# Performance work log

Hardware: AMD Instinct MI355X
Metric: run time of the kernel (lower is better)

The kernel has to match this reference:

```python
import jax, jax.numpy as jnp
import numpy as np

# Dims: B=batch, N_IN=input capsules, D_IN=input capsule dim,
#       J=output capsules (nb_capsules), C=output capsule dim (capsule_size)
B, N_IN, D_IN, J, C = 32, 2048, 16, 64, 32
ITERS = 5
EPS = 1e-7  # K.epsilon()


def squash(v):
    # Keras code: vector += eps; norm = sum(v^2, -1, keepdims); v * norm/(1+norm)/sqrt(norm)
    v = v + EPS
    n = jnp.sum(v * v, axis=-1, keepdims=True)
    return v * (n / (1.0 + n) / jnp.sqrt(n))


def setup_inputs() -> dict:
    key = jax.random.key(0)
    k1, k2 = jax.random.split(key)
    x = jax.random.normal(k1, (B, N_IN, D_IN, 1), dtype=jnp.float32)
    # glorot_uniform over fan_in=D_IN (last axis), fan_out=C
    limit = float(np.sqrt(6.0 / (D_IN + C)))
    W = jax.random.uniform(k2, (N_IN, J, C, D_IN), dtype=jnp.float32,
                           minval=-limit, maxval=limit)
    return {"x": x, "W": W}


def reference(x, W):
    # x: (B, N_IN, D_IN, 1) -> u: (B, N_IN, D_IN)
    u = x[..., 0]
    # Prediction vectors u_hat[b,i,j] = W[i,j] @ u[b,i] : (B, N_IN, J, C)
    u_hat = jnp.einsum('bid,ijcd->bijc', u, W)
    # Routing logits b_ij: (B, N_IN, J)
    b = jnp.zeros(u_hat.shape[:3], dtype=u_hat.dtype)
    v = None
    for i in range(ITERS):
        c = jax.nn.softmax(b, axis=1)              # softmax over input capsules (axis=1 in source)
        s = jnp.einsum('bij,bijc->bjc', c, u_hat)   # weighted sum over i -> (B, J, C)
        v = squash(s)                                # squash over capsule vector dim C
        if i < ITERS - 1:
            # agreement update: b += <v_j, u_hat_ij>
            b = b + jnp.einsum('bjc,bijc->bij', v, u_hat)
    # match compute_output_shape (B, nb_capsules, capsule_size, 1)
    return v[..., None]
```

## Files before the change

kernel.cpp:

```cpp
#include <hip/hip_runtime.h>
#include <hip/hip_bf16.h>

#define B_ 32
#define N_ 2048
#define D_ 16
#define J_ 64
#define C_ 32
#define NCHUNK 32
#define ICHUNK 64
#define IPW    16

typedef __attribute__((ext_vector_type(8)))  short short8;
typedef __attribute__((ext_vector_type(4)))  short s16x4;
typedef __attribute__((ext_vector_type(16))) float f32x16;
typedef __attribute__((ext_vector_type(4)))  float f32x4;

using bf16_t = __hip_bfloat16;

__global__ __launch_bounds__(256) void prep_u_kernel(const float* __restrict__ x,
                                                     bf16_t* __restrict__ ut) {
  int t  = blockIdx.x * 256 + threadIdx.x;
  int d4 = t & 3;
  int bi = t >> 2;
  int b  = bi & 31;
  int i  = bi >> 5;
  f32x4 xv = *(const f32x4*)(x + ((size_t)(b * N_ + i) * D_ + d4 * 4));
  union { s16x4 v; bf16_t h[4]; } o;
  o.h[0] = __float2bfloat16(xv.x);
  o.h[1] = __float2bfloat16(xv.y);
  o.h[2] = __float2bfloat16(xv.z);
  o.h[3] = __float2bfloat16(xv.w);
  *(s16x4*)(ut + (size_t)(i * B_ + b) * D_ + d4 * 4) = o.v;
}

template<int MODE>
__global__ __launch_bounds__(256) void pass_kernel(
    const float*  __restrict__ Wf,
    const bf16_t* __restrict__ Wb,
    bf16_t*       __restrict__ Wbo,
    const bf16_t* __restrict__ ut,
    const float*  __restrict__ V,
    float*        __restrict__ PS,
    float*        __restrict__ PZ)
{
  constexpr bool UNIFORM = (MODE == 0 || MODE == 2);
  constexpr bool READF32 = (MODE != 1);
  constexpr bool STOREB  = (MODE == 0);

  const int tid  = threadIdx.x;
  const int w    = tid >> 6;
  const int lane = tid & 63;
  const int half = lane >> 5;
  const int lc   = lane & 31;

  const int j  = blockIdx.x / NCHUNK;
  const int ch = blockIdx.x % NCHUNK;

  int crow[16];
#pragma unroll
  for (int r = 0; r < 16; ++r) crow[r] = (r & 3) + 4 * half + 8 * (r >> 2);

  float Vreg[16];
  if (!UNIFORM) {
#pragma unroll
    for (int r = 0; r < 16; ++r) Vreg[r] = V[(lc * J_ + j) * C_ + crow[r]];
  }

  float S[16];
#pragma unroll
  for (int r = 0; r < 16; ++r) S[r] = 0.f;
  float zacc = 0.f;

  const int ibase = ch * ICHUNK + w * IPW;
  const int frag_off = lc * D_ + half * 8;

  const f32x16 zeroacc = {0,0,0,0,0,0,0,0,0,0,0,0,0,0,0,0};

  for (int t = 0; t < IPW; ++t) {
    const int i = ibase + t;
    short8 ufrag = *(const short8*)(ut + (size_t)i * (B_ * D_) + frag_off);
    short8 wfrag;
    const size_t tile = ((size_t)i * J_ + j) * (C_ * D_);
    if (READF32) {
      const float* wp = Wf + tile + frag_off;
      f32x4 w0 = *(const f32x4*)(wp);
      f32x4 w1 = *(const f32x4*)(wp + 4);
      union { short8 v; bf16_t h[8]; } cv;
      cv.h[0] = __float2bfloat16(w0.x);
      cv.h[1] = __float2bfloat16(w0.y);
      cv.h[2] = __float2bfloat16(w0.z);
      cv.h[3] = __float2bfloat16(w0.w);
      cv.h[4] = __float2bfloat16(w1.x);
      cv.h[5] = __float2bfloat16(w1.y);
      cv.h[6] = __float2bfloat16(w1.z);
      cv.h[7] = __float2bfloat16(w1.w);
      wfrag = cv.v;
      if (STOREB) *(short8*)(Wbo + tile + frag_off) = wfrag;
    } else {
      wfrag = *(const short8*)(Wb + tile + frag_off);
    }

    f32x16 acc = __builtin_amdgcn_mfma_f32_32x32x16_bf16(wfrag, ufrag, zeroacc, 0, 0, 0);

    if (UNIFORM) {
#pragma unroll
      for (int r = 0; r < 16; ++r) S[r] += acc[r];
    } else {
      float ph = 0.f;
#pragma unroll
      for (int r = 0; r < 16; ++r) ph = fmaf(Vreg[r], acc[r], ph);
      ph += __shfl_xor(ph, 32);
      float e = __expf(ph);
      zacc += e;
#pragma unroll
      for (int r = 0; r < 16; ++r) S[r] = fmaf(e, acc[r], S[r]);
    }
  }

  __shared__ float S_lds[4 * 32 * 33];
  __shared__ float Z_lds[4 * 32];
#pragma unroll
  for (int r = 0; r < 16; ++r)
    S_lds[w * 1056 + lc * 33 + crow[r]] = S[r];
  if (!half)
    Z_lds[w * 32 + lc] = UNIFORM ? (float)IPW : zacc;
  __syncthreads();

  const size_t pbase = (size_t)blockIdx.x * 1024;
  for (int e = tid; e < 1024; e += 256) {
    int b = e >> 5, c = e & 31;
    PS[pbase + e] = S_lds[b * 33 + c] + S_lds[1056 + b * 33 + c] +
                    S_lds[2112 + b * 33 + c] + S_lds[3168 + b * 33 + c];
  }
  if (tid < 32)
    PZ[(size_t)blockIdx.x * 32 + tid] =
        Z_lds[tid] + Z_lds[32 + tid] + Z_lds[64 + tid] + Z_lds[96 + tid];
}

__global__ __launch_bounds__(256) void combine_kernel(
    const float* __restrict__ PS, const float* __restrict__ PZ,
    float* __restrict__ V, float* __restrict__ out, int first, int last)
{
  int t  = blockIdx.x * 256 + threadIdx.x;
  int c  = t & 31;
  int bj = t >> 5;
  int b  = bj >> 6;
  int j  = bj & 63;
  float s = 0.f, zz = 0.f;
#pragma unroll
  for (int ch = 0; ch < NCHUNK; ++ch) {
    s  += PS[(size_t)(j * NCHUNK + ch) * 1024 + b * 32 + c];
    zz += PZ[(j * NCHUNK + ch) * 32 + b];
  }
  float sv = s / zz + 1e-7f;
  float n = sv * sv;
  n += __shfl_xor(n, 1);
  n += __shfl_xor(n, 2);
  n += __shfl_xor(n, 4);
  n += __shfl_xor(n, 8);
  n += __shfl_xor(n, 16);
  float f = n / ((1.f + n) * sqrtf(n));
  float v = sv * f;
  float Vn = first ? v : (V[t] + v);
  V[t] = Vn;
  if (last) out[t] = v;
}

extern "C" void kernel_launch(void* const* d_in, const int* in_sizes, int n_in,
                              void* d_out, int out_size, void* d_ws, size_t ws_size,
                              hipStream_t stream)
{
  const float* x  = (const float*)d_in[0];
  const float* Wf = (const float*)d_in[1];
  float* out = (float*)d_out;
  char* ws = (char*)d_ws;

  const size_t SZ_WB = (size_t)N_ * J_ * C_ * D_ * 2;
  const size_t SZ_UT = (size_t)N_ * B_ * D_ * 2;
  const size_t SZ_V  = (size_t)B_ * J_ * C_ * 4;
  const size_t SZ_PS = (size_t)J_ * NCHUNK * B_ * C_ * 4;
  const size_t SZ_PZ = (size_t)J_ * NCHUNK * B_ * 4;

  const bool big = ws_size >= SZ_WB + SZ_UT + SZ_V + SZ_PS + SZ_PZ;
  size_t off = big ? SZ_WB : 0;
  bf16_t* Wb = (bf16_t*)ws;
  bf16_t* ut = (bf16_t*)(ws + off); off += SZ_UT;
  float*  V  = (float*)(ws + off);  off += SZ_V;
  float*  PS = (float*)(ws + off);  off += SZ_PS;
  float*  PZ = (float*)(ws + off);

  prep_u_kernel<<<dim3((N_ * B_ * 4) / 256), dim3(256), 0, stream>>>(x, ut);

  dim3 gA(J_ * NCHUNK), blk(256), gB((B_ * J_ * C_) / 256);
  if (big) {
    pass_kernel<0><<<gA, blk, 0, stream>>>(Wf, nullptr, Wb, ut, nullptr, PS, PZ);
    combine_kernel<<<gB, blk, 0, stream>>>(PS, PZ, V, out, 1, 0);
    for (int it = 1; it < 5; ++it) {
      pass_kernel<1><<<gA, blk, 0, stream>>>(nullptr, Wb, nullptr, ut, V, PS, PZ);
      combine_kernel<<<gB, blk, 0, stream>>>(PS, PZ, V, out, 0, it == 4 ? 1 : 0);
    }
  } else {
    pass_kernel<2><<<gA, blk, 0, stream>>>(Wf, nullptr, nullptr, ut, nullptr, PS, PZ);
    combine_kernel<<<gB, blk, 0, stream>>>(PS, PZ, V, out, 1, 0);
    for (int it = 1; it < 5; ++it) {
      pass_kernel<3><<<gA, blk, 0, stream>>>(Wf, nullptr, nullptr, ut, V, PS, PZ);
      combine_kernel<<<gB, blk, 0, stream>>>(PS, PZ, V, out, 0, it == 4 ? 1 : 0);
    }
  }
}
```

Measured before the change: 512.5 us.

## Quantize W and u to int8 with per-tile scales and use i8 MFMA

The first pass now quantizes each W[i,j] 32x16 tile to int8 with a per-tile absmax scale and stores it to the workspace. The prep kernel quantizes each u[b,i] vector to int8 with a per-vector scale. Later routing passes stream the int8 weights, half the bytes of the previous bf16 copy, run i8 MFMA, and rescale the accumulators in fp32. This targets the memory-bandwidth cost of re-reading W every iteration, in exchange for lower precision and extra scale loads and conversions.

```diff
diff --git a/kernel.cpp b/kernel.cpp
--- a/kernel.cpp
+++ b/kernel.cpp
@@ -14,38 +14,59 @@
 typedef __attribute__((ext_vector_type(4)))  short s16x4;
 typedef __attribute__((ext_vector_type(16))) float f32x16;
 typedef __attribute__((ext_vector_type(4)))  float f32x4;
+typedef __attribute__((ext_vector_type(16))) int   i32x16;
+typedef __attribute__((ext_vector_type(2)))  long  longx2;
 
 using bf16_t = __hip_bfloat16;
 
 __global__ __launch_bounds__(256) void prep_u_kernel(const float* __restrict__ x,
-                                                     bf16_t* __restrict__ ut) {
-  int t  = blockIdx.x * 256 + threadIdx.x;
-  int d4 = t & 3;
-  int bi = t >> 2;
-  int b  = bi & 31;
-  int i  = bi >> 5;
-  f32x4 xv = *(const f32x4*)(x + ((size_t)(b * N_ + i) * D_ + d4 * 4));
-  union { s16x4 v; bf16_t h[4]; } o;
-  o.h[0] = __float2bfloat16(xv.x);
-  o.h[1] = __float2bfloat16(xv.y);
-  o.h[2] = __float2bfloat16(xv.z);
-  o.h[3] = __float2bfloat16(xv.w);
-  *(s16x4*)(ut + (size_t)(i * B_ + b) * D_ + d4 * 4) = o.v;
+                                                     bf16_t* __restrict__ ut,
+                                                     signed char* __restrict__ uq,
+                                                     float* __restrict__ su) {
+  int t = blockIdx.x * 256 + threadIdx.x;
+  int b = t & 31;
+  int i = t >> 5;
+  const float* xp = x + (size_t)(b * N_ + i) * D_;
+  float v[16];
+  *(f32x4*)(v)      = *(const f32x4*)(xp);
+  *(f32x4*)(v + 4)  = *(const f32x4*)(xp + 4);
+  *(f32x4*)(v + 8)  = *(const f32x4*)(xp + 8);
+  *(f32x4*)(v + 12) = *(const f32x4*)(xp + 12);
+
+  float m = 0.f;
+#pragma unroll
+  for (int k = 0; k < 16; ++k) m = fmaxf(m, fabsf(v[k]));
+  m = fmaxf(m, 1e-20f);
+  float inv = 127.0f / m;
+  union { longx2 l2; signed char c[16]; } pk;
+#pragma unroll
+  for (int k = 0; k < 16; ++k) pk.c[k] = (signed char)__float2int_rn(v[k] * inv);
+  *(longx2*)(uq + (size_t)t * D_) = pk.l2;
+  su[t] = m * (1.0f / 127.0f);
+
+  union { short8 s; bf16_t h[8]; } o0, o1;
+#pragma unroll
+  for (int k = 0; k < 8; ++k) { o0.h[k] = __float2bfloat16(v[k]); o1.h[k] = __float2bfloat16(v[8 + k]); }
+  *(short8*)(ut + (size_t)t * D_)     = o0.s;
+  *(short8*)(ut + (size_t)t * D_ + 8) = o1.s;
 }
 
 template<int MODE>
 __global__ __launch_bounds__(256) void pass_kernel(
-    const float*  __restrict__ Wf,
-    const bf16_t* __restrict__ Wb,
-    bf16_t*       __restrict__ Wbo,
-    const bf16_t* __restrict__ ut,
-    const float*  __restrict__ V,
-    float*        __restrict__ PS,
-    float*        __restrict__ PZ)
+    const float*        __restrict__ Wf,
+    const signed char*  __restrict__ Wq,
+    signed char*        __restrict__ Wqo,
+    float*              __restrict__ SWo,
+    const float*        __restrict__ SW,
+    const signed char*  __restrict__ uq,
+    const float*        __restrict__ su,
+    const bf16_t*       __restrict__ ut,
+    const float*        __restrict__ V,
+    float*              __restrict__ PS,
+    float*              __restrict__ PZ)
 {
   constexpr bool UNIFORM = (MODE == 0 || MODE == 2);
-  constexpr bool READF32 = (MODE != 1);
-  constexpr bool STOREB  = (MODE == 0);
+  constexpr bool INT8    = (MODE == 0 || MODE == 1);
 
   const int tid  = threadIdx.x;
   const int w    = tid >> 6;
@@ -74,14 +95,68 @@
   const int ibase = ch * ICHUNK + w * IPW;
   const int frag_off = lc * D_ + half * 8;
 
-  const f32x16 zeroacc = {0,0,0,0,0,0,0,0,0,0,0,0,0,0,0,0};
-
-  for (int t = 0; t < IPW; ++t) {
-    const int i = ibase + t;
-    short8 ufrag = *(const short8*)(ut + (size_t)i * (B_ * D_) + frag_off);
-    short8 wfrag;
-    const size_t tile = ((size_t)i * J_ + j) * (C_ * D_);
-    if (READF32) {
+  if constexpr (INT8) {
+    const i32x16 zi = {0,0,0,0,0,0,0,0,0,0,0,0,0,0,0,0};
+    for (int t = 0; t < IPW; ++t) {
+      const int i = ibase + t;
+      long ul = *(const long*)(uq + (size_t)i * (B_ * D_) + frag_off);
+      const size_t tile = ((size_t)i * J_ + j) * (C_ * D_);
+      long wl;
+      float sw_i;
+      if constexpr (MODE == 0) {
+        const float* wp = Wf + tile + frag_off;
+        f32x4 w0 = *(const f32x4*)(wp);
+        f32x4 w1 = *(const f32x4*)(wp + 4);
+        float wv[8] = {w0.x, w0.y, w0.z, w0.w, w1.x, w1.y, w1.z, w1.w};
+        float m = 0.f;
+#pragma unroll
+        for (int k = 0; k < 8; ++k) m = fmaxf(m, fabsf(wv[k]));
+        m = fmaxf(m, __shfl_xor(m, 1));
+        m = fmaxf(m, __shfl_xor(m, 2));
+        m = fmaxf(m, __shfl_xor(m, 4));
+        m = fmaxf(m, __shfl_xor(m, 8));
+        m = fmaxf(m, __shfl_xor(m, 16));
+        m = fmaxf(m, __shfl_xor(m, 32));
+        m = fmaxf(m, 1e-20f);
+        float qs = 127.0f / m;
+        union { long l; signed char c[8]; } pk;
+#pragma unroll
+        for (int k = 0; k < 8; ++k) pk.c[k] = (signed char)__float2int_rn(wv[k] * qs);
+        wl = pk.l;
+        sw_i = m * (1.0f / 127.0f);
+        *(long*)(Wqo + tile + frag_off) = wl;
+        if (lane == 0) SWo[(size_t)i * J_ + j] = sw_i;
+      } else {
+        wl = *(const long*)(Wq + tile + frag_off);
+        sw_i = SW[(size_t)i * J_ + j];
+      }
+      const float s = sw_i * su[i * B_ + lc];
+
+      i32x16 iacc = __builtin_amdgcn_mfma_i32_32x32x16_i8(wl, ul, zi, 0, 0, 0);
+
+      if constexpr (UNIFORM) {
+#pragma unroll
+        for (int r = 0; r < 16; ++r) S[r] = fmaf(s, (float)iacc[r], S[r]);
+      } else {
+        float af[16];
+        float ph = 0.f;
+#pragma unroll
+        for (int r = 0; r < 16; ++r) { af[r] = (float)iacc[r]; ph = fmaf(Vreg[r], af[r], ph); }
+        ph *= s;
+        ph += __shfl_xor(ph, 32);
+        float e = __expf(ph);
+        zacc += e;
+        float es = e * s;
+#pragma unroll
+        for (int r = 0; r < 16; ++r) S[r] = fmaf(es, af[r], S[r]);
+      }
+    }
+  } else {
+    const f32x16 zeroacc = {0,0,0,0,0,0,0,0,0,0,0,0,0,0,0,0};
+    for (int t = 0; t < IPW; ++t) {
+      const int i = ibase + t;
+      short8 ufrag = *(const short8*)(ut + (size_t)i * (B_ * D_) + frag_off);
+      const size_t tile = ((size_t)i * J_ + j) * (C_ * D_);
       const float* wp = Wf + tile + frag_off;
       f32x4 w0 = *(const f32x4*)(wp);
       f32x4 w1 = *(const f32x4*)(wp + 4);
@@ -94,26 +169,23 @@
       cv.h[5] = __float2bfloat16(w1.y);
       cv.h[6] = __float2bfloat16(w1.z);
       cv.h[7] = __float2bfloat16(w1.w);
-      wfrag = cv.v;
-      if (STOREB) *(short8*)(Wbo + tile + frag_off) = wfrag;
-    } else {
-      wfrag = *(const short8*)(Wb + tile + frag_off);
-    }
-
-    f32x16 acc = __builtin_amdgcn_mfma_f32_32x32x16_bf16(wfrag, ufrag, zeroacc, 0, 0, 0);
-
-    if (UNIFORM) {
-#pragma unroll
-      for (int r = 0; r < 16; ++r) S[r] += acc[r];
-    } else {
-      float ph = 0.f;
-#pragma unroll
-      for (int r = 0; r < 16; ++r) ph = fmaf(Vreg[r], acc[r], ph);
-      ph += __shfl_xor(ph, 32);
-      float e = __expf(ph);
-      zacc += e;
-#pragma unroll
-      for (int r = 0; r < 16; ++r) S[r] = fmaf(e, acc[r], S[r]);
+      short8 wfrag = cv.v;
+
+      f32x16 acc = __builtin_amdgcn_mfma_f32_32x32x16_bf16(wfrag, ufrag, zeroacc, 0, 0, 0);
+
+      if constexpr (UNIFORM) {
+#pragma unroll
+        for (int r = 0; r < 16; ++r) S[r] += acc[r];
+      } else {
+        float ph = 0.f;
+#pragma unroll
+        for (int r = 0; r < 16; ++r) ph = fmaf(Vreg[r], acc[r], ph);
+        ph += __shfl_xor(ph, 32);
+        float e = __expf(ph);
+        zacc += e;
+#pragma unroll
+        for (int r = 0; r < 16; ++r) S[r] = fmaf(e, acc[r], S[r]);
+      }
     }
   }
 
@@ -175,35 +247,45 @@
   float* out = (float*)d_out;
   char* ws = (char*)d_ws;
 
-  const size_t SZ_WB = (size_t)N_ * J_ * C_ * D_ * 2;
+  const size_t SZ_WQ = (size_t)N_ * J_ * C_ * D_;
+  const size_t SZ_SW = (size_t)N_ * J_ * 4;
+  const size_t SZ_UQ = (size_t)N_ * B_ * D_;
+  const size_t SZ_SU = (size_t)N_ * B_ * 4;
   const size_t SZ_UT = (size_t)N_ * B_ * D_ * 2;
   const size_t SZ_V  = (size_t)B_ * J_ * C_ * 4;
   const size_t SZ_PS = (size_t)J_ * NCHUNK * B_ * C_ * 4;
   const size_t SZ_PZ = (size_t)J_ * NCHUNK * B_ * 4;
 
-  const bool big = ws_size >= SZ_WB + SZ_UT + SZ_V + SZ_PS + SZ_PZ;
-  size_t off = big ? SZ_WB : 0;
-  bf16_t* Wb = (bf16_t*)ws;
-  bf16_t* ut = (bf16_t*)(ws + off); off += SZ_UT;
-  float*  V  = (float*)(ws + off);  off += SZ_V;
-  float*  PS = (float*)(ws + off);  off += SZ_PS;
-  float*  PZ = (float*)(ws + off);
-
-  prep_u_kernel<<<dim3((N_ * B_ * 4) / 256), dim3(256), 0, stream>>>(x, ut);
+  const bool big = ws_size >= SZ_WQ + SZ_SW + SZ_UQ + SZ_SU + SZ_UT + SZ_V + SZ_PS + SZ_PZ;
+  char* p = ws;
+  signed char* Wq = nullptr;
+  float* SWp = nullptr;
+  if (big) {
+    Wq  = (signed char*)p; p += SZ_WQ;
+    SWp = (float*)p;       p += SZ_SW;
+  }
+  signed char* uq = (signed char*)p; p += SZ_UQ;
+  float* su = (float*)p;             p += SZ_SU;
+  bf16_t* ut = (bf16_t*)p;           p += SZ_UT;
+  float*  V  = (float*)p;            p += SZ_V;
+  float*  PS = (float*)p;            p += SZ_PS;
+  float*  PZ = (float*)p;
+
+  prep_u_kernel<<<dim3((N_ * B_) / 256), dim3(256), 0, stream>>>(x, ut, uq, su);
 
   dim3 gA(J_ * NCHUNK), blk(256), gB((B_ * J_ * C_) / 256);
   if (big) {
-    pass_kernel<0><<<gA, blk, 0, stream>>>(Wf, nullptr, Wb, ut, nullptr, PS, PZ);
+    pass_kernel<0><<<gA, blk, 0, stream>>>(Wf, nullptr, Wq, SWp, nullptr, uq, su, ut, nullptr, PS, PZ);
     combine_kernel<<<gB, blk, 0, stream>>>(PS, PZ, V, out, 1, 0);
     for (int it = 1; it < 5; ++it) {
-      pass_kernel<1><<<gA, blk, 0, stream>>>(nullptr, Wb, nullptr, ut, V, PS, PZ);
+      pass_kernel<1><<<gA, blk, 0, stream>>>(nullptr, Wq, nullptr, nullptr, SWp, uq, su, ut, V, PS, PZ);
       combine_kernel<<<gB, blk, 0, stream>>>(PS, PZ, V, out, 0, it == 4 ? 1 : 0);
     }
   } else {
-    pass_kernel<2><<<gA, blk, 0, stream>>>(Wf, nullptr, nullptr, ut, nullptr, PS, PZ);
+    pass_kernel<2><<<gA, blk, 0, stream>>>(Wf, nullptr, nullptr, nullptr, nullptr, uq, su, ut, nullptr, PS, PZ);
     combine_kernel<<<gB, blk, 0, stream>>>(PS, PZ, V, out, 1, 0);
     for (int it = 1; it < 5; ++it) {
-      pass_kernel<3><<<gA, blk, 0, stream>>>(Wf, nullptr, nullptr, ut, V, PS, PZ);
+      pass_kernel<3><<<gA, blk, 0, stream>>>(Wf, nullptr, nullptr, nullptr, nullptr, uq, su, ut, V, PS, PZ);
       combine_kernel<<<gB, blk, 0, stream>>>(PS, PZ, V, out, 0, it == 4 ? 1 : 0);
     }
   }
```

New measurement: 513.9 us. Within noise of the previous version (+0.3%).
